# Kernel tuning notes

Measured on AMD Instinct MI355X. Metric: run time of the kernel, lower is better.

The kernel has to match this reference:

```python
import jax, jax.numpy as jnp
import numpy as np
import itertools

N = 600000
CIN = 64
COUT = 64
KS = 3
STRIDE = 2
DIL = 1
GRID = 256        # coordinate range before striding
M = 512           # per-axis key radix (fits int32 keys for batch<=2)
SHIFT = (KS - 1) // 2 * DIL   # keeps shifted coords non-negative under neighbor offsets
SENT = 2 ** 30    # sentinel key for padded unique slots
BN_EPS = 1e-5

OFFSETS = list(itertools.product(range(-(KS // 2), KS // 2 + 1), repeat=3))  # 27 offsets, row-major


def setup_inputs() -> dict:
    key = jax.random.key(0)
    k1, k2, k3, k4, k5, k6, k7, k8 = jax.random.split(key, 8)
    xyz = jax.random.randint(k1, (N, 3), 0, GRID, dtype=jnp.int32)
    b = jax.random.randint(k2, (N, 1), 0, 2, dtype=jnp.int32)  # batch of 2 scenes
    coords = jnp.concatenate([xyz, b], axis=1)                 # [N,4] = (x,y,z,batch)
    feats = jax.random.normal(k3, (N, CIN), dtype=jnp.float32)
    weight = jax.random.normal(k4, (27, CIN, COUT), dtype=jnp.float32) / np.sqrt(27 * CIN)
    bn_scale = jax.random.uniform(k5, (COUT,), jnp.float32, 0.5, 1.5)
    bn_bias = jax.random.normal(k6, (COUT,), jnp.float32) * 0.1
    bn_mean = jax.random.normal(k7, (COUT,), jnp.float32) * 0.1
    bn_var = jax.random.uniform(k8, (COUT,), jnp.float32, 0.5, 1.5)
    return {"coords": coords, "feats": feats, "weight": weight,
            "bn_scale": bn_scale, "bn_bias": bn_bias, "bn_mean": bn_mean, "bn_var": bn_var}


def _encode(xyz, b):
    # pack (batch, x, y, z) into a single sortable int32 key
    return ((b * M + xyz[:, 0] + SHIFT) * M + (xyz[:, 1] + SHIFT)) * M + (xyz[:, 2] + SHIFT)


def _forward(coords, feats, weight, bn_scale, bn_bias, bn_mean, bn_var):
    # --- stride path: voxel downsample via unique + scatter-add (index_add) ---
    xyz = coords[:, :3] // STRIDE
    b = coords[:, 3]
    keys = _encode(xyz, b)                                   # [N]
    ukeys, inv = jnp.unique(keys, size=N, fill_value=SENT, return_inverse=True)  # sorted, padded
    fds = jax.ops.segment_sum(feats, inv, num_segments=N)    # pooled feats [N, CIN]
    valid = ukeys < SENT                                      # real (non-padded) voxels

    # --- sparse 3x3x3 conv at stride 1 (output coords == input coords) ---
    # gather(neighbor) -> matmul(W_k) -> accumulate, per kernel offset
    out = jnp.zeros((N, COUT), dtype=feats.dtype)
    for k, (dx, dy, dz) in enumerate(OFFSETS):
        delta = ((dx * M) + dy) * M + dz
        q = ukeys + delta * DIL
        pos = jnp.clip(jnp.searchsorted(ukeys, q), 0, N - 1)
        match = (ukeys[pos] == q) & valid
        gathered = jnp.where(match[:, None], fds[pos], 0.0)   # [N, CIN]
        out = out + gathered @ weight[k]

    # --- BatchNorm (eval-mode running stats) + ReLU ---
    inv_std = jax.lax.rsqrt(bn_var + BN_EPS)
    out = (out - bn_mean) * (bn_scale * inv_std) + bn_bias
    out = jax.nn.relu(out)
    return jnp.where(valid[:, None], out, 0.0)                # zero padded rows


def reference(coords, feats, weight, bn_scale, bn_bias, bn_mean, bn_var):
    return _forward(coords, feats, weight, bn_scale, bn_bias, bn_mean, bn_var)
```

## Files before the change

kernel.cpp:

```cpp
#include <hip/hip_runtime.h>
#include <hip/hip_bf16.h>

#define NPTS 600000
#define NKEYS (1 << 22)
#define CHUNK 4096
#define NPART (NKEYS / CHUNK)

typedef unsigned int u32;
typedef unsigned short u16;
typedef __attribute__((ext_vector_type(8))) short short8;
typedef __attribute__((ext_vector_type(4))) int i32x4;
typedef __attribute__((ext_vector_type(4))) float f32x4;

__device__ __forceinline__ u16 f2bf(float x) {
  union { float f; u32 u; } c; c.f = x;
  u32 r = c.u + 0x7fffu + ((c.u >> 16) & 1u);
  return (u16)(r >> 16);
}

__global__ void k0a_bn(const float* __restrict__ s, const float* __restrict__ b,
                       const float* __restrict__ m, const float* __restrict__ v,
                       float* __restrict__ ab) {
  int c = threadIdx.x;
  float a = s[c] * rsqrtf(v[c] + 1e-5f);
  ab[c] = a;
  ab[64 + c] = b[c] - m[c] * a;
}

__global__ void k0b_wt(const float* __restrict__ W, u16* __restrict__ Wt) {
  int e = blockIdx.x * 256 + threadIdx.x;
  if (e >= 27 * 4096) return;
  int k = e >> 12, rem = e & 4095, cin = rem >> 6, cout = rem & 63;
  Wt[(k << 12) + (cout << 6) + cin] = f2bf(W[e]);
}

__global__ void k1_keys(const int* __restrict__ coords, int* __restrict__ keys,
                        u32* __restrict__ lut) {
  int i = blockIdx.x * 256 + threadIdx.x;
  if (i >= NPTS) return;
  int4 c4 = *(const int4*)(coords + i * 4);
  int k = (c4.w << 21) | ((c4.x >> 1) << 14) | ((c4.y >> 1) << 7) | (c4.z >> 1);
  keys[i] = k;
  atomicAdd(&lut[k], 1u);
}

__global__ void k2a_part(const u32* __restrict__ lut, u32* __restrict__ partials) {
  __shared__ u32 sd[256];
  int blk = blockIdx.x, t = threadIdx.x;
  const u32* p = lut + blk * CHUNK;
  u32 s = 0;
  for (int j = t; j < CHUNK; j += 256) s += (p[j] != 0u);
  sd[t] = s; __syncthreads();
  for (int o = 128; o > 0; o >>= 1) { if (t < o) sd[t] += sd[t + o]; __syncthreads(); }
  if (t == 0) partials[blk] = sd[0];
}

__global__ void k2b_top(u32* __restrict__ partials) {
  __shared__ u32 sh[NPART];
  int t = threadIdx.x;
  u32 x = partials[t];
  sh[t] = x; __syncthreads();
  for (int off = 1; off < NPART; off <<= 1) {
    u32 add = (t >= off) ? sh[t - off] : 0u;
    __syncthreads();
    sh[t] += add;
    __syncthreads();
  }
  partials[t] = sh[t] - x;
  if (t == NPART - 1) partials[NPART] = sh[t];
}

__global__ void k2c_fill(u32* __restrict__ lut, const u32* __restrict__ partials,
                         int* __restrict__ r2k, float* __restrict__ fds32) {
  __shared__ u32 tsum[256];
  int blk = blockIdx.x, t = threadIdx.x;
  int base = blk * CHUNK + t * 16;
  u32 loc[16]; u32 s = 0;
#pragma unroll
  for (int j = 0; j < 16; j++) { loc[j] = lut[base + j]; s += (loc[j] != 0u); }
  tsum[t] = s; __syncthreads();
  for (int off = 1; off < 256; off <<= 1) {
    u32 add = (t >= off) ? tsum[t - off] : 0u;
    __syncthreads();
    tsum[t] += add;
    __syncthreads();
  }
  u32 rank = partials[blk] + tsum[t] - s;
#pragma unroll
  for (int j = 0; j < 16; j++) {
    if (loc[j]) {
      u32 flag = (loc[j] > 1u) ? 0x80000000u : 0u;
      lut[base + j] = (rank + 1u) | flag;
      r2k[rank] = base + j;
      if (flag) {
        float4 z = {0.f, 0.f, 0.f, 0.f};
        float* d = fds32 + ((size_t)rank << 6);
#pragma unroll
        for (int c = 0; c < 16; c++) *(float4*)(d + c * 4) = z;
      }
      rank++;
    } else lut[base + j] = 0u;
  }
}

__global__ void k3_seg(const float* __restrict__ feats, const int* __restrict__ keys,
                       const u32* __restrict__ lut, float* __restrict__ fds32,
                       u16* __restrict__ fdsb) {
  int idx = blockIdx.x * 256 + threadIdx.x;
  if (idx >= NPTS * 16) return;
  int i = idx >> 4, q = (idx & 15) << 2;
  u32 lv = lut[keys[i]];
  u32 r = (lv & 0x7fffffffu) - 1u;
  float4 v = *(const float4*)(feats + (size_t)i * 64 + q);
  if (lv >> 31) {
    float* dst = fds32 + ((size_t)r << 6) + q;
    atomicAdd(dst + 0, v.x); atomicAdd(dst + 1, v.y);
    atomicAdd(dst + 2, v.z); atomicAdd(dst + 3, v.w);
  } else {
    ushort4 o;
    o.x = f2bf(v.x); o.y = f2bf(v.y); o.z = f2bf(v.z); o.w = f2bf(v.w);
    *(ushort4*)(fdsb + ((size_t)r << 6) + q) = o;
  }
}

__global__ void k3b_fix(const int* __restrict__ r2k, const u32* __restrict__ lut,
                        const u32* __restrict__ pU,
                        const float* __restrict__ fds32, u16* __restrict__ fdsb) {
  int idx = blockIdx.x * 256 + threadIdx.x;
  int r = idx >> 2;
  if (r >= (int)(*pU)) return;
  u32 lv = lut[r2k[r]];
  if (!(lv >> 31)) return;
  int q = (idx & 3) << 4;
  const float* src = fds32 + ((size_t)r << 6) + q;
  u16* dst = fdsb + ((size_t)r << 6) + q;
#pragma unroll
  for (int j = 0; j < 4; j++) {
    float4 v = *(const float4*)(src + j * 4);
    ushort4 o;
    o.x = f2bf(v.x); o.y = f2bf(v.y); o.z = f2bf(v.z); o.w = f2bf(v.w);
    *(ushort4*)(dst + j * 4) = o;
  }
}

__global__ __launch_bounds__(256) void k4_conv(
    const u32* __restrict__ lut, const int* __restrict__ r2k,
    const u16* __restrict__ fdsb, const u16* __restrict__ Wt,
    const u32* __restrict__ pU, const float* __restrict__ ab,
    float* __restrict__ out) {
  __shared__ __align__(16) char ldsA[2][8192];
  const u32 U = *pU;
  int tid = threadIdx.x;
  int w = tid >> 6, l = tid & 63;
  int bid = blockIdx.x;
  int nwg = (int)gridDim.x, q = nwg >> 3, rr = nwg & 7;
  int xcd = bid & 7, t8 = bid >> 3;
  int swz = (xcd < rr ? xcd * (q + 1) : rr * (q + 1) + (xcd - rr) * q) + t8;
  int rbase = swz * 64;

  int lr = (w << 4) + (l >> 2);
  int col = l & 15, kg = l >> 4;

  int key = -1, x = 0, y = 0, z = 0;
  {
    int r = rbase + lr;
    key = ((u32)r < U) ? r2k[r] : -1;
    z = key & 127; y = (key >> 7) & 127; x = (key >> 14) & 127;
  }

  u32 lvr[4];
  i32x4 rgA[3][2];
  i32x4 bB[3][2];
  f32x4 acc[4] = {};

#define P_(T) { \
    const int dx_ = (T) / 9 - 1, dy_ = ((T) / 3) % 3 - 1, dz_ = (T) % 3 - 1; \
    int nx_ = x + dx_, ny_ = y + dy_, nz_ = z + dz_; \
    bool ok_ = (key >= 0) & ((u32)nx_ < 128u) & ((u32)ny_ < 128u) & ((u32)nz_ < 128u); \
    const u32* pp_ = lut + (ok_ ? (key + dx_ * 16384 + dy_ * 128 + dz_) : NKEYS); \
    asm volatile("global_load_dword %0, %1, off" \
                 : "=&v"(lvr[(T) & 3]) : "v"(pp_) : "memory"); }

#define L_(T) { \
    u32 lv_ = lvr[(T) & 3]; \
    u32 row_ = lv_ ? ((lv_ & 0x7fffffffu) - 1u) : (u32)NPTS; \
    const char* fr_ = (const char*)(fdsb + ((size_t)row_ << 6)) + ((l & 3) << 5); \
    asm volatile("global_load_dwordx4 %0, %1, off" \
                 : "=&v"(rgA[(T) % 3][0]) : "v"(fr_) : "memory"); \
    asm volatile("global_load_dwordx4 %0, %1, off offset:16" \
                 : "=&v"(rgA[(T) % 3][1]) : "v"(fr_) : "memory"); }

#define B_(T) { \
    const u16* wb_ = Wt + ((T) << 12) + (((w << 4) + col) << 6) + (kg << 3); \
    asm volatile("global_load_dwordx4 %0, %1, off" \
                 : "=&v"(bB[(T) % 3][0]) : "v"(wb_) : "memory"); \
    asm volatile("global_load_dwordx4 %0, %1, off offset:64" \
                 : "=&v"(bB[(T) % 3][1]) : "v"(wb_) : "memory"); }

#define DSW_(T) { \
    char* dst_ = &ldsA[(T) & 1][lr * 128]; \
    int r7_ = lr & 7, c0_ = (l & 3) << 1; \
    *(i32x4*)(dst_ + (((c0_ + r7_) & 7) << 4))     = rgA[(T) % 3][0]; \
    *(i32x4*)(dst_ + (((c0_ + 1 + r7_) & 7) << 4)) = rgA[(T) % 3][1]; }

#define CONSUME(K) { \
    short8 b0_ = *(short8*)&bB[(K) % 3][0]; \
    short8 b1_ = *(short8*)&bB[(K) % 3][1]; \
    const char* slab_ = &ldsA[(K) & 1][0]; \
    _Pragma("unroll") for (int rt = 0; rt < 4; rt++) { \
      int row_ = (rt << 4) + col; \
      const char* rp_ = slab_ + row_ * 128; \
      int r7_ = row_ & 7; \
      short8 a0_ = *(const short8*)(rp_ + (((kg + r7_) & 7) << 4)); \
      short8 a1_ = *(const short8*)(rp_ + (((kg + 4 + r7_) & 7) << 4)); \
      acc[rt] = __builtin_amdgcn_mfma_f32_16x16x32_bf16(a0_, b0_, acc[rt], 0, 0, 0); \
      acc[rt] = __builtin_amdgcn_mfma_f32_16x16x32_bf16(a1_, b1_, acc[rt], 0, 0, 0); } }

#define WAITC(N) { asm volatile("s_waitcnt vmcnt(%0)" :: "n"(N) : "memory"); \
                   __builtin_amdgcn_sched_barrier(0); }
#define BAR() { \
    asm volatile("" ::: "memory"); \
    asm volatile("s_waitcnt lgkmcnt(0)" ::: "memory"); \
    __builtin_amdgcn_s_barrier(); \
    asm volatile("" ::: "memory"); }

  P_(0) P_(1) P_(2)
  WAITC(0)
  L_(0) L_(1) P_(3) B_(0) B_(1)
  WAITC(7)
  DSW_(0)
  P_(4) L_(2)
  BAR()

#define NW(K) (2 * ((K) + 1 < 27) + 2 * ((K) + 2 < 27) + 1 * ((K) + 4 < 27))
#define BODY(K) { \
    WAITC(NW(K)) \
    if ((K) + 1 < 27) DSW_((K) + 1) \
    if ((K) + 3 < 27) L_((K) + 3) \
    if ((K) + 5 < 27) P_((K) + 5) \
    if ((K) + 2 < 27) B_((K) + 2) \
    CONSUME(K) \
    BAR() }

  BODY(0)  BODY(1)  BODY(2)  BODY(3)  BODY(4)  BODY(5)  BODY(6)
  BODY(7)  BODY(8)  BODY(9)  BODY(10) BODY(11) BODY(12) BODY(13)
  BODY(14) BODY(15) BODY(16) BODY(17) BODY(18) BODY(19) BODY(20)
  BODY(21) BODY(22) BODY(23) BODY(24) BODY(25) BODY(26)

#undef P_
#undef L_
#undef B_
#undef DSW_
#undef CONSUME
#undef WAITC
#undef BAR
#undef NW
#undef BODY

  {
    int c = (w << 4) | col;
    float al = ab[c], be = ab[64 + c];
#pragma unroll
    for (int rt = 0; rt < 4; rt++) {
#pragma unroll
      for (int i = 0; i < 4; i++) {
        int r = rbase + (rt << 4) + (kg << 2) + i;
        if (r >= NPTS) continue;
        bool valid = ((u32)r < U);
        float vv = 0.f;
        if (valid) {
          vv = fmaf(acc[rt][i], al, be);
          vv = vv > 0.f ? vv : 0.f;
        }
        out[((size_t)r << 6) + c] = vv;
      }
    }
  }
}

extern "C" void kernel_launch(void* const* d_in, const int* in_sizes, int n_in,
                              void* d_out, int out_size, void* d_ws, size_t ws_size,
                              hipStream_t stream) {
  const int*   coords = (const int*)d_in[0];
  const float* feats  = (const float*)d_in[1];
  const float* W      = (const float*)d_in[2];
  const float* bns    = (const float*)d_in[3];
  const float* bnb    = (const float*)d_in[4];
  const float* bnm    = (const float*)d_in[5];
  const float* bnv    = (const float*)d_in[6];
  float* out = (float*)d_out;

  char* ws = (char*)d_ws;
  size_t off = 0;
  auto alloc = [&](size_t bytes) -> void* {
    void* p = ws + off;
    off += (bytes + 255) & ~(size_t)255;
    return p;
  };
  u32* lut      = (u32*)alloc((size_t)(NKEYS + 1) * 4);
  u32* partials = (u32*)alloc((NPART + 8) * 4);
  int* keys     = (int*)alloc((size_t)NPTS * 4);
  int* r2k      = (int*)alloc((size_t)NPTS * 4);
  u16* fdsb     = (u16*)alloc((size_t)(NPTS + 1) * 64 * 2);
  u16* Wt       = (u16*)alloc((size_t)27 * 4096 * 2);
  float* ab     = (float*)alloc(128 * 4);
  (void)ws_size; (void)out_size; (void)n_in; (void)in_sizes;

  float* fds32 = out;

  hipMemsetAsync(lut, 0, (size_t)(NKEYS + 1) * 4, stream);
  hipMemsetAsync(fdsb + (size_t)NPTS * 64, 0, 128, stream);

  k0a_bn<<<1, 64, 0, stream>>>(bns, bnb, bnm, bnv, ab);
  k0b_wt<<<(27 * 4096 + 255) / 256, 256, 0, stream>>>(W, Wt);
  k1_keys<<<(NPTS + 255) / 256, 256, 0, stream>>>(coords, keys, lut);
  k2a_part<<<NPART, 256, 0, stream>>>(lut, partials);
  k2b_top<<<1, NPART, 0, stream>>>(partials);
  k2c_fill<<<NPART, 256, 0, stream>>>(lut, partials, r2k, fds32);
  k3_seg<<<(NPTS * 16 + 255) / 256, 256, 0, stream>>>(feats, keys, lut, fds32, fdsb);
  k3b_fix<<<(NPTS * 4 + 255) / 256, 256, 0, stream>>>(r2k, lut, partials + NPART, fds32, fdsb);
  k4_conv<<<(NPTS + 63) / 64, 256, 0, stream>>>(lut, r2k, fdsb, Wt,
                                                partials + NPART, ab, out);
}
```

Baseline: 477.4 us.

## Add occupancy bitmap for neighbor probes and fuse chunk counting into key atomics

```diff
diff --git a/kernel.cpp b/kernel.cpp
--- a/kernel.cpp
+++ b/kernel.cpp
@@ -3,6 +3,7 @@
 
 #define NPTS 600000
 #define NKEYS (1 << 22)
+#define NWORDS (NKEYS >> 5)
 #define CHUNK 4096
 #define NPART (NKEYS / CHUNK)
 
@@ -35,24 +36,14 @@
 }
 
 __global__ void k1_keys(const int* __restrict__ coords, int* __restrict__ keys,
-                        u32* __restrict__ lut) {
+                        u32* __restrict__ lut, u32* __restrict__ partials) {
   int i = blockIdx.x * 256 + threadIdx.x;
   if (i >= NPTS) return;
   int4 c4 = *(const int4*)(coords + i * 4);
   int k = (c4.w << 21) | ((c4.x >> 1) << 14) | ((c4.y >> 1) << 7) | (c4.z >> 1);
   keys[i] = k;
-  atomicAdd(&lut[k], 1u);
-}
-
-__global__ void k2a_part(const u32* __restrict__ lut, u32* __restrict__ partials) {
-  __shared__ u32 sd[256];
-  int blk = blockIdx.x, t = threadIdx.x;
-  const u32* p = lut + blk * CHUNK;
-  u32 s = 0;
-  for (int j = t; j < CHUNK; j += 256) s += (p[j] != 0u);
-  sd[t] = s; __syncthreads();
-  for (int o = 128; o > 0; o >>= 1) { if (t < o) sd[t] += sd[t + o]; __syncthreads(); }
-  if (t == 0) partials[blk] = sd[0];
+  u32 old = atomicAdd(&lut[k], 1u);
+  if (old == 0u) atomicAdd(&partials[k >> 12], 1u);
 }
 
 __global__ void k2b_top(u32* __restrict__ partials) {
@@ -71,13 +62,21 @@
 }
 
 __global__ void k2c_fill(u32* __restrict__ lut, const u32* __restrict__ partials,
-                         int* __restrict__ r2k, float* __restrict__ fds32) {
+                         int* __restrict__ r2k, float* __restrict__ fds32,
+                         u32* __restrict__ bmw) {
   __shared__ u32 tsum[256];
   int blk = blockIdx.x, t = threadIdx.x;
   int base = blk * CHUNK + t * 16;
   u32 loc[16]; u32 s = 0;
 #pragma unroll
   for (int j = 0; j < 16; j++) { loc[j] = lut[base + j]; s += (loc[j] != 0u); }
+  {
+    u32 m16 = 0;
+#pragma unroll
+    for (int j = 0; j < 16; j++) m16 |= (loc[j] != 0u) << j;
+    u32 other = __shfl_xor(m16, 1);
+    if (!(t & 1)) bmw[blk * 128 + (t >> 1)] = m16 | (other << 16);
+  }
   tsum[t] = s; __syncthreads();
   for (int off = 1; off < 256; off <<= 1) {
     u32 add = (t >= off) ? tsum[t - off] : 0u;
@@ -147,7 +146,7 @@
     const u32* __restrict__ lut, const int* __restrict__ r2k,
     const u16* __restrict__ fdsb, const u16* __restrict__ Wt,
     const u32* __restrict__ pU, const float* __restrict__ ab,
-    float* __restrict__ out) {
+    const u32* __restrict__ bmw, float* __restrict__ out) {
   __shared__ __align__(16) char ldsA[2][8192];
   const u32 U = *pU;
   int tid = threadIdx.x;
@@ -159,6 +158,7 @@
   int rbase = swz * 64;
 
   int lr = (w << 4) + (l >> 2);
+  int bo = (l & 3) << 5;
   int col = l & 15, kg = l >> 4;
 
   int key = -1, x = 0, y = 0, z = 0;
@@ -168,23 +168,35 @@
     z = key & 127; y = (key >> 7) & 127; x = (key >> 14) & 127;
   }
 
+  u32 lvw[8];
   u32 lvr[4];
   i32x4 rgA[3][2];
   i32x4 bB[3][2];
   f32x4 acc[4] = {};
 
-#define P_(T) { \
+#define OKBASE(T) \
     const int dx_ = (T) / 9 - 1, dy_ = ((T) / 3) % 3 - 1, dz_ = (T) % 3 - 1; \
     int nx_ = x + dx_, ny_ = y + dy_, nz_ = z + dz_; \
     bool ok_ = (key >= 0) & ((u32)nx_ < 128u) & ((u32)ny_ < 128u) & ((u32)nz_ < 128u); \
-    const u32* pp_ = lut + (ok_ ? (key + dx_ * 16384 + dy_ * 128 + dz_) : NKEYS); \
+    int base_ = key + dx_ * 16384 + dy_ * 128 + dz_;
+
+#define W_(T) { \
+    OKBASE(T) \
+    const u32* wp_ = bmw + (ok_ ? ((u32)base_ >> 5) : (u32)NWORDS); \
     asm volatile("global_load_dword %0, %1, off" \
-                 : "=&v"(lvr[(T) & 3]) : "v"(pp_) : "memory"); }
+                 : "=&v"(lvw[(T) & 7]) : "v"(wp_) : "memory"); }
+
+#define R_(T) { \
+    OKBASE(T) \
+    u32 hit_ = ok_ ? ((lvw[(T) & 7] >> ((u32)base_ & 31u)) & 1u) : 0u; \
+    const u32* rp_ = lut + (hit_ ? (u32)base_ : (u32)NKEYS); \
+    asm volatile("global_load_dword %0, %1, off" \
+                 : "=&v"(lvr[(T) & 3]) : "v"(rp_) : "memory"); }
 
 #define L_(T) { \
     u32 lv_ = lvr[(T) & 3]; \
     u32 row_ = lv_ ? ((lv_ & 0x7fffffffu) - 1u) : (u32)NPTS; \
-    const char* fr_ = (const char*)(fdsb + ((size_t)row_ << 6)) + ((l & 3) << 5); \
+    const char* fr_ = (const char*)(fdsb + ((size_t)row_ << 6)) + bo; \
     asm volatile("global_load_dwordx4 %0, %1, off" \
                  : "=&v"(rgA[(T) % 3][0]) : "v"(fr_) : "memory"); \
     asm volatile("global_load_dwordx4 %0, %1, off offset:16" \
@@ -224,20 +236,25 @@
     __builtin_amdgcn_s_barrier(); \
     asm volatile("" ::: "memory"); }
 
-  P_(0) P_(1) P_(2)
+  W_(0) W_(1) W_(2) W_(3) W_(4)
   WAITC(0)
-  L_(0) L_(1) P_(3) B_(0) B_(1)
-  WAITC(7)
+  R_(0) R_(1) R_(2)
+  WAITC(0)
+  L_(0)
+  WAITC(0)
   DSW_(0)
-  P_(4) L_(2)
+  L_(1) R_(3) W_(5) B_(0)
+  L_(2) R_(4) W_(6) B_(1)
   BAR()
 
-#define NW(K) (2 * ((K) + 1 < 27) + 2 * ((K) + 2 < 27) + 1 * ((K) + 4 < 27))
+#define NW(K) (2 * ((K) + 2 < 27) + 1 * ((K) + 4 < 27) + \
+               1 * ((K) + 6 < 27) + 2 * ((K) + 1 < 27))
 #define BODY(K) { \
     WAITC(NW(K)) \
     if ((K) + 1 < 27) DSW_((K) + 1) \
     if ((K) + 3 < 27) L_((K) + 3) \
-    if ((K) + 5 < 27) P_((K) + 5) \
+    if ((K) + 5 < 27) R_((K) + 5) \
+    if ((K) + 7 < 27) W_((K) + 7) \
     if ((K) + 2 < 27) B_((K) + 2) \
     CONSUME(K) \
     BAR() }
@@ -247,7 +264,9 @@
   BODY(14) BODY(15) BODY(16) BODY(17) BODY(18) BODY(19) BODY(20)
   BODY(21) BODY(22) BODY(23) BODY(24) BODY(25) BODY(26)
 
-#undef P_
+#undef OKBASE
+#undef W_
+#undef R_
 #undef L_
 #undef B_
 #undef DSW_
@@ -304,21 +323,23 @@
   u16* fdsb     = (u16*)alloc((size_t)(NPTS + 1) * 64 * 2);
   u16* Wt       = (u16*)alloc((size_t)27 * 4096 * 2);
   float* ab     = (float*)alloc(128 * 4);
+  u32* bmw      = (u32*)alloc((size_t)(NWORDS + 64) * 4);
   (void)ws_size; (void)out_size; (void)n_in; (void)in_sizes;
 
   float* fds32 = out;
 
   hipMemsetAsync(lut, 0, (size_t)(NKEYS + 1) * 4, stream);
+  hipMemsetAsync(partials, 0, (NPART + 8) * 4, stream);
   hipMemsetAsync(fdsb + (size_t)NPTS * 64, 0, 128, stream);
+  hipMemsetAsync(bmw + NWORDS, 0, 64 * 4, stream);
 
   k0a_bn<<<1, 64, 0, stream>>>(bns, bnb, bnm, bnv, ab);
   k0b_wt<<<(27 * 4096 + 255) / 256, 256, 0, stream>>>(W, Wt);
-  k1_keys<<<(NPTS + 255) / 256, 256, 0, stream>>>(coords, keys, lut);
-  k2a_part<<<NPART, 256, 0, stream>>>(lut, partials);
+  k1_keys<<<(NPTS + 255) / 256, 256, 0, stream>>>(coords, keys, lut, partials);
   k2b_top<<<1, NPART, 0, stream>>>(partials);
-  k2c_fill<<<NPART, 256, 0, stream>>>(lut, partials, r2k, fds32);
+  k2c_fill<<<NPART, 256, 0, stream>>>(lut, partials, r2k, fds32, bmw);
   k3_seg<<<(NPTS * 16 + 255) / 256, 256, 0, stream>>>(feats, keys, lut, fds32, fdsb);
   k3b_fix<<<(NPTS * 4 + 255) / 256, 256, 0, stream>>>(r2k, lut, partials + NPART, fds32, fdsb);
   k4_conv<<<(NPTS + 63) / 64, 256, 0, stream>>>(lut, r2k, fdsb, Wt,
-                                                partials + NPART, ab, out);
-}
+                                                partials + NPART, ab, bmw, out);
+}
```

Measured after the change: 597.1 us. 1.25x slower.

## Retile conv waves to 2x2 MFMA blocks and fuse chunk counting into key pass

Applied to the files above, without the earlier changes.

```diff
diff --git a/kernel.cpp b/kernel.cpp
--- a/kernel.cpp
+++ b/kernel.cpp
@@ -35,24 +35,14 @@
 }
 
 __global__ void k1_keys(const int* __restrict__ coords, int* __restrict__ keys,
-                        u32* __restrict__ lut) {
+                        u32* __restrict__ lut, u32* __restrict__ partials) {
   int i = blockIdx.x * 256 + threadIdx.x;
   if (i >= NPTS) return;
   int4 c4 = *(const int4*)(coords + i * 4);
   int k = (c4.w << 21) | ((c4.x >> 1) << 14) | ((c4.y >> 1) << 7) | (c4.z >> 1);
   keys[i] = k;
-  atomicAdd(&lut[k], 1u);
-}
-
-__global__ void k2a_part(const u32* __restrict__ lut, u32* __restrict__ partials) {
-  __shared__ u32 sd[256];
-  int blk = blockIdx.x, t = threadIdx.x;
-  const u32* p = lut + blk * CHUNK;
-  u32 s = 0;
-  for (int j = t; j < CHUNK; j += 256) s += (p[j] != 0u);
-  sd[t] = s; __syncthreads();
-  for (int o = 128; o > 0; o >>= 1) { if (t < o) sd[t] += sd[t + o]; __syncthreads(); }
-  if (t == 0) partials[blk] = sd[0];
+  u32 old = atomicAdd(&lut[k], 1u);
+  if (old == 0u) atomicAdd(&partials[k >> 12], 1u);
 }
 
 __global__ void k2b_top(u32* __restrict__ partials) {
@@ -159,7 +149,9 @@
   int rbase = swz * 64;
 
   int lr = (w << 4) + (l >> 2);
+  int bo = (l & 3) << 5;
   int col = l & 15, kg = l >> 4;
+  int wi = w >> 1, wj = w & 1;
 
   int key = -1, x = 0, y = 0, z = 0;
   {
@@ -170,8 +162,8 @@
 
   u32 lvr[4];
   i32x4 rgA[3][2];
-  i32x4 bB[3][2];
-  f32x4 acc[4] = {};
+  i32x4 bB[3][4];
+  f32x4 acc[2][2] = {};
 
 #define P_(T) { \
     const int dx_ = (T) / 9 - 1, dy_ = ((T) / 3) % 3 - 1, dz_ = (T) % 3 - 1; \
@@ -184,18 +176,22 @@
 #define L_(T) { \
     u32 lv_ = lvr[(T) & 3]; \
     u32 row_ = lv_ ? ((lv_ & 0x7fffffffu) - 1u) : (u32)NPTS; \
-    const char* fr_ = (const char*)(fdsb + ((size_t)row_ << 6)) + ((l & 3) << 5); \
+    const char* fr_ = (const char*)(fdsb + ((size_t)row_ << 6)) + bo; \
     asm volatile("global_load_dwordx4 %0, %1, off" \
                  : "=&v"(rgA[(T) % 3][0]) : "v"(fr_) : "memory"); \
     asm volatile("global_load_dwordx4 %0, %1, off offset:16" \
                  : "=&v"(rgA[(T) % 3][1]) : "v"(fr_) : "memory"); }
 
 #define B_(T) { \
-    const u16* wb_ = Wt + ((T) << 12) + (((w << 4) + col) << 6) + (kg << 3); \
+    const u16* wb_ = Wt + ((T) << 12) + (((wj << 5) + col) << 6) + (kg << 3); \
     asm volatile("global_load_dwordx4 %0, %1, off" \
                  : "=&v"(bB[(T) % 3][0]) : "v"(wb_) : "memory"); \
     asm volatile("global_load_dwordx4 %0, %1, off offset:64" \
-                 : "=&v"(bB[(T) % 3][1]) : "v"(wb_) : "memory"); }
+                 : "=&v"(bB[(T) % 3][1]) : "v"(wb_) : "memory"); \
+    asm volatile("global_load_dwordx4 %0, %1, off offset:2048" \
+                 : "=&v"(bB[(T) % 3][2]) : "v"(wb_) : "memory"); \
+    asm volatile("global_load_dwordx4 %0, %1, off offset:2112" \
+                 : "=&v"(bB[(T) % 3][3]) : "v"(wb_) : "memory"); }
 
 #define DSW_(T) { \
     char* dst_ = &ldsA[(T) & 1][lr * 128]; \
@@ -204,17 +200,21 @@
     *(i32x4*)(dst_ + (((c0_ + 1 + r7_) & 7) << 4)) = rgA[(T) % 3][1]; }
 
 #define CONSUME(K) { \
-    short8 b0_ = *(short8*)&bB[(K) % 3][0]; \
-    short8 b1_ = *(short8*)&bB[(K) % 3][1]; \
+    short8 b00_ = *(short8*)&bB[(K) % 3][0]; \
+    short8 b01_ = *(short8*)&bB[(K) % 3][1]; \
+    short8 b10_ = *(short8*)&bB[(K) % 3][2]; \
+    short8 b11_ = *(short8*)&bB[(K) % 3][3]; \
     const char* slab_ = &ldsA[(K) & 1][0]; \
-    _Pragma("unroll") for (int rt = 0; rt < 4; rt++) { \
-      int row_ = (rt << 4) + col; \
+    _Pragma("unroll") for (int rt = 0; rt < 2; rt++) { \
+      int row_ = (wi << 5) + (rt << 4) + col; \
       const char* rp_ = slab_ + row_ * 128; \
       int r7_ = row_ & 7; \
       short8 a0_ = *(const short8*)(rp_ + (((kg + r7_) & 7) << 4)); \
       short8 a1_ = *(const short8*)(rp_ + (((kg + 4 + r7_) & 7) << 4)); \
-      acc[rt] = __builtin_amdgcn_mfma_f32_16x16x32_bf16(a0_, b0_, acc[rt], 0, 0, 0); \
-      acc[rt] = __builtin_amdgcn_mfma_f32_16x16x32_bf16(a1_, b1_, acc[rt], 0, 0, 0); } }
+      acc[rt][0] = __builtin_amdgcn_mfma_f32_16x16x32_bf16(a0_, b00_, acc[rt][0], 0, 0, 0); \
+      acc[rt][0] = __builtin_amdgcn_mfma_f32_16x16x32_bf16(a1_, b01_, acc[rt][0], 0, 0, 0); \
+      acc[rt][1] = __builtin_amdgcn_mfma_f32_16x16x32_bf16(a0_, b10_, acc[rt][1], 0, 0, 0); \
+      acc[rt][1] = __builtin_amdgcn_mfma_f32_16x16x32_bf16(a1_, b11_, acc[rt][1], 0, 0, 0); } }
 
 #define WAITC(N) { asm volatile("s_waitcnt vmcnt(%0)" :: "n"(N) : "memory"); \
                    __builtin_amdgcn_sched_barrier(0); }
@@ -226,13 +226,14 @@
 
   P_(0) P_(1) P_(2)
   WAITC(0)
-  L_(0) L_(1) P_(3) B_(0) B_(1)
-  WAITC(7)
+  L_(0)
+  WAITC(0)
   DSW_(0)
-  P_(4) L_(2)
+  L_(1) P_(3) B_(0)
+  L_(2) P_(4) B_(1)
   BAR()
 
-#define NW(K) (2 * ((K) + 1 < 27) + 2 * ((K) + 2 < 27) + 1 * ((K) + 4 < 27))
+#define NW(K) (2 * ((K) + 2 < 27) + 1 * ((K) + 4 < 27) + 4 * ((K) + 1 < 27))
 #define BODY(K) { \
     WAITC(NW(K)) \
     if ((K) + 1 < 27) DSW_((K) + 1) \
@@ -258,21 +259,24 @@
 #undef BODY
 
   {
-    int c = (w << 4) | col;
-    float al = ab[c], be = ab[64 + c];
-#pragma unroll
-    for (int rt = 0; rt < 4; rt++) {
-#pragma unroll
-      for (int i = 0; i < 4; i++) {
-        int r = rbase + (rt << 4) + (kg << 2) + i;
-        if (r >= NPTS) continue;
-        bool valid = ((u32)r < U);
-        float vv = 0.f;
-        if (valid) {
-          vv = fmaf(acc[rt][i], al, be);
-          vv = vv > 0.f ? vv : 0.f;
+#pragma unroll
+    for (int ct = 0; ct < 2; ct++) {
+      int c = (wj << 5) + (ct << 4) + col;
+      float al = ab[c], be = ab[64 + c];
+#pragma unroll
+      for (int rt = 0; rt < 2; rt++) {
+#pragma unroll
+        for (int i = 0; i < 4; i++) {
+          int r = rbase + (wi << 5) + (rt << 4) + (kg << 2) + i;
+          if (r >= NPTS) continue;
+          bool valid = ((u32)r < U);
+          float vv = 0.f;
+          if (valid) {
+            vv = fmaf(acc[rt][ct][i], al, be);
+            vv = vv > 0.f ? vv : 0.f;
+          }
+          out[((size_t)r << 6) + c] = vv;
         }
-        out[((size_t)r << 6) + c] = vv;
       }
     }
   }
@@ -309,12 +313,12 @@
   float* fds32 = out;
 
   hipMemsetAsync(lut, 0, (size_t)(NKEYS + 1) * 4, stream);
+  hipMemsetAsync(partials, 0, (NPART + 8) * 4, stream);
   hipMemsetAsync(fdsb + (size_t)NPTS * 64, 0, 128, stream);
 
   k0a_bn<<<1, 64, 0, stream>>>(bns, bnb, bnm, bnv, ab);
   k0b_wt<<<(27 * 4096 + 255) / 256, 256, 0, stream>>>(W, Wt);
-  k1_keys<<<(NPTS + 255) / 256, 256, 0, stream>>>(coords, keys, lut);
-  k2a_part<<<NPART, 256, 0, stream>>>(lut, partials);
+  k1_keys<<<(NPTS + 255) / 256, 256, 0, stream>>>(coords, keys, lut, partials);
   k2b_top<<<1, NPART, 0, stream>>>(partials);
   k2c_fill<<<NPART, 256, 0, stream>>>(lut, partials, r2k, fds32);
   k3_seg<<<(NPTS * 16 + 255) / 256, 256, 0, stream>>>(feats, keys, lut, fds32, fdsb);
```

After: 801.2 us. 1.68x slower.
